# Kernel optimization log

Measured on AMD Instinct MI355X. Metric: run time of the kernel, lower is better.

The kernel has to match this reference:

```python
import jax, jax.numpy as jnp
import numpy as np

NEG = -1e9  # mask value for non-edges (matches masked_fill(-inf) numerically-safely)
SLOPE = 0.2  # LeakyReLU negative slope in GraphAttentionLayer


def gat_layer(x, W, a_l, a_r, adj, n_heads):
    """One GraphAttentionLayer (eval mode, is_concat=True).
    e[i,j,h] = leakyrelu(a_l . g[i,h] + a_r . g[j,h])  (attn Linear split into halves)
    softmax over j masked by adj, then aggregate neighbors.
    """
    n = x.shape[0]
    g = (x @ W).reshape(n, n_heads, -1)          # [n, h, f]
    el = jnp.einsum('ihf,f->ih', g, a_l)          # score contribution of node i
    er = jnp.einsum('jhf,f->jh', g, a_r)          # score contribution of node j
    e = jax.nn.leaky_relu(el[:, None, :] + er[None, :, :], SLOPE)  # [n, n, h]
    e = jnp.where(adj[:, :, None] != 0, e, NEG)
    a = jax.nn.softmax(e, axis=1)                 # softmax over neighbors j
    out = jnp.einsum('ijh,jhf->ihf', a, g)        # weighted aggregation
    return out.reshape(n, -1)                     # concat heads


def setup_inputs() -> dict:
    key = jax.random.key(0)
    ks = jax.random.split(key, 8)
    N, IN, HID, OUT, H = 2048, 512, 256, 128, 8
    x = jax.random.normal(ks[0], (N, IN), dtype=jnp.float32)
    adj = jax.random.randint(ks[1], (N, N), 0, 2, dtype=jnp.int32)
    adj = adj.at[jnp.arange(N), jnp.arange(N)].set(1)  # self loops: no empty softmax rows
    s = 0.05
    W1 = jax.random.normal(ks[2], (IN, HID), dtype=jnp.float32) * s
    a1_l = jax.random.normal(ks[3], (HID // H,), dtype=jnp.float32) * s
    a1_r = jax.random.normal(ks[4], (HID // H,), dtype=jnp.float32) * s
    W2 = jax.random.normal(ks[5], (HID, OUT), dtype=jnp.float32) * s
    a2_l = jax.random.normal(ks[6], (OUT,), dtype=jnp.float32) * s
    a2_r = jax.random.normal(ks[7], (OUT,), dtype=jnp.float32) * s
    return {"x": x, "W1": W1, "a1_l": a1_l, "a1_r": a1_r,
            "W2": W2, "a2_l": a2_l, "a2_r": a2_r, "adj_mat": adj}


def reference(x, W1, a1_l, a1_r, W2, a2_l, a2_r, adj_mat):
    # eval mode: nn.Dropout is identity
    h = gat_layer(x, W1, a1_l, a1_r, adj_mat, n_heads=8)
    h = jax.nn.elu(h)
    out = gat_layer(h, W2, a2_l, a2_r, adj_mat, n_heads=1)
    return out
```

## Files before the change

kernel.cpp:

```cpp
#include <hip/hip_runtime.h>
#include <hip/hip_bf16.h>

#define NN 2048
typedef unsigned short u16;
typedef unsigned long long u64;
typedef __attribute__((ext_vector_type(8))) short short8;
typedef __attribute__((ext_vector_type(4))) float f32x4;

__device__ __forceinline__ unsigned bfb(float x) {
    unsigned u = __float_as_uint(x);
    return (u + 0x7FFFu + ((u >> 16) & 1u)) >> 16;
}
__device__ __forceinline__ unsigned pk2(float a, float b) { return bfb(a) | (bfb(b) << 16); }

__global__ __launch_bounds__(256) void prep(const float* __restrict__ x,
                                            const float* __restrict__ W1,
                                            const float* __restrict__ W2,
                                            const int* __restrict__ adj,
                                            u16* __restrict__ xb, u16* __restrict__ w1t,
                                            u16* __restrict__ w2t, u64* __restrict__ ab) {
    const int b = blockIdx.x;
    if (b < 16384) {
        int t = b * 256 + threadIdx.x;
        int W = t >> 6, lane = t & 63;
        int i = W >> 5, jw = W & 31;
        int a = adj[(size_t)i * NN + jw * 64 + lane];
        u64 m = __ballot(a != 0);
        if (lane == 0) ab[(size_t)i * 32 + jw] = m;
    } else if (b < 16384 + 1024) {
        int t = (b - 16384) * 256 + threadIdx.x;
        float4 v = ((const float4*)x)[t];
        uint2 o;
        o.x = pk2(v.x, v.y);
        o.y = pk2(v.z, v.w);
        ((uint2*)xb)[t] = o;
    } else if (b < 16384 + 1024 + 512) {
        int u = (b - 17408) * 256 + threadIdx.x;
        int c = u >> 9, k = u & 511;
        w1t[u] = (u16)bfb(W1[(size_t)k * 256 + c]);
    } else {
        int u = (b - 17920) * 256 + threadIdx.x;
        int c = u >> 8, k = u & 255;
        w2t[u] = (u16)bfb(W2[(size_t)k * 128 + c]);
    }
}

__global__ __launch_bounds__(256) void gemm1(const u16* __restrict__ A,
                                             const u16* __restrict__ BT,
                                             const float* __restrict__ al,
                                             const float* __restrict__ ar,
                                             u16* __restrict__ GT,
                                             float* __restrict__ el,
                                             float* __restrict__ ert) {
    const int i0 = blockIdx.x * 16, cs = blockIdx.y;
    const int t = threadIdx.x, lane = t & 63, w = t >> 6;
    const int q = lane >> 4, n = lane & 15;
    const int ct = w & 1, kh = w >> 1;
    __shared__ float osh[2][16][16];
    __shared__ float pel[2][16], per_[2][16];

    const u16* ap = A + (size_t)(i0 + n) * 512 + kh * 256 + q * 8;
    const u16* bp = BT + (size_t)(cs * 32 + ct * 16 + n) * 512 + kh * 256 + q * 8;
    f32x4 acc = {0.f, 0.f, 0.f, 0.f};
#pragma unroll
    for (int ks = 0; ks < 8; ++ks) {
        short8 a = *(const short8*)(ap + ks * 32);
        short8 b = *(const short8*)(bp + ks * 32);
        acc = __builtin_amdgcn_mfma_f32_16x16x32_bf16(a, b, acc, 0, 0, 0);
    }
    if (kh == 1) {
#pragma unroll
        for (int r = 0; r < 4; ++r) osh[ct][q * 4 + r][n] = acc[r];
    }
    __syncthreads();
    if (kh == 0) {
#pragma unroll
        for (int r = 0; r < 4; ++r) acc[r] += osh[ct][q * 4 + r][n];
        uint2 g0;
        g0.x = pk2(acc[0], acc[1]);
        g0.y = pk2(acc[2], acc[3]);
        *(uint2*)&GT[(size_t)(cs * 32 + ct * 16 + n) * NN + i0 + q * 4] = g0;
        const float alv = al[ct * 16 + n], arv = ar[ct * 16 + n];
#pragma unroll
        for (int r = 0; r < 4; ++r) {
            float ve = acc[r] * alv, vr = acc[r] * arv;
#pragma unroll
            for (int off = 1; off <= 8; off <<= 1) {
                ve += __shfl_xor(ve, off);
                vr += __shfl_xor(vr, off);
            }
            if (n == 0) { pel[ct][q * 4 + r] = ve; per_[ct][q * 4 + r] = vr; }
        }
    }
    __syncthreads();
    if (t < 16) {
        el[(size_t)(i0 + t) * 8 + cs] = pel[0][t] + pel[1][t];
        ert[(size_t)cs * NN + i0 + t] = per_[0][t] + per_[1][t];
    }
}

__global__ __launch_bounds__(256) void gemm2(const u16* __restrict__ A,
                                             const u16* __restrict__ BT,
                                             const float* __restrict__ al,
                                             const float* __restrict__ ar,
                                             u16* __restrict__ GT,
                                             float* __restrict__ el2p,
                                             float* __restrict__ er2p) {
    const int i0 = blockIdx.x * 16, cs = blockIdx.y;
    const int t = threadIdx.x, lane = t & 63, w = t >> 6;
    const int q = lane >> 4, n = lane & 15;
    const int ct = w & 1, kh = w >> 1;
    __shared__ float osh[2][16][16];
    __shared__ float pel[2][16], per_[2][16];

    const u16* ap = A + (size_t)(i0 + n) * 256 + kh * 128 + q * 8;
    const u16* bp = BT + (size_t)(cs * 32 + ct * 16 + n) * 256 + kh * 128 + q * 8;
    f32x4 acc = {0.f, 0.f, 0.f, 0.f};
#pragma unroll
    for (int ks = 0; ks < 4; ++ks) {
        short8 a = *(const short8*)(ap + ks * 32);
        short8 b = *(const short8*)(bp + ks * 32);
        acc = __builtin_amdgcn_mfma_f32_16x16x32_bf16(a, b, acc, 0, 0, 0);
    }
    if (kh == 1) {
#pragma unroll
        for (int r = 0; r < 4; ++r) osh[ct][q * 4 + r][n] = acc[r];
    }
    __syncthreads();
    if (kh == 0) {
#pragma unroll
        for (int r = 0; r < 4; ++r) acc[r] += osh[ct][q * 4 + r][n];
        uint2 g0;
        g0.x = pk2(acc[0], acc[1]);
        g0.y = pk2(acc[2], acc[3]);
        *(uint2*)&GT[(size_t)(cs * 32 + ct * 16 + n) * NN + i0 + q * 4] = g0;
        const float alv = al[cs * 32 + ct * 16 + n], arv = ar[cs * 32 + ct * 16 + n];
#pragma unroll
        for (int r = 0; r < 4; ++r) {
            float ve = acc[r] * alv, vr = acc[r] * arv;
#pragma unroll
            for (int off = 1; off <= 8; off <<= 1) {
                ve += __shfl_xor(ve, off);
                vr += __shfl_xor(vr, off);
            }
            if (n == 0) { pel[ct][q * 4 + r] = ve; per_[ct][q * 4 + r] = vr; }
        }
    }
    __syncthreads();
    if (t < 16) {
        el2p[(size_t)cs * NN + i0 + t] = pel[0][t] + pel[1][t];
        er2p[(size_t)cs * NN + i0 + t] = per_[0][t] + per_[1][t];
    }
}

__global__ __launch_bounds__(512) void attn1(const float* __restrict__ el,
                                             const float* __restrict__ ert,
                                             const unsigned* __restrict__ ab32,
                                             const u16* __restrict__ gbt,
                                             u16* __restrict__ hbb) {
    const int rt = blockIdx.x, sec = blockIdx.y;
    const int i0 = rt * 16, h0 = sec * 2;
    const int t = threadIdx.x, lane = t & 63, w = t >> 6;
    const int q = lane >> 4, n = lane & 15;
    const int m = t >> 5, jq = t & 31;
    const int hl = w >> 2, ch = (w >> 1) & 1, kf2 = w & 1;

    __shared__ u16 ersb[2][2048];
    __shared__ __align__(16) u16 pl[2][2][16][136];
    __shared__ unsigned absh[16][64];
    __shared__ float psum_sh[16][2];
    __shared__ float osh[2][2][16][16];
    __shared__ float wmax[2][8];
    __shared__ float mxsh[2];

    float4 v0 = *(const float4*)(ert + (size_t)h0 * NN + t * 4);
    float4 v1 = *(const float4*)(ert + (size_t)(h0 + 1) * NN + t * 4);
    uint2 c0, c1;
    c0.x = pk2(v0.x, v0.y); c0.y = pk2(v0.z, v0.w);
    c1.x = pk2(v1.x, v1.y); c1.y = pk2(v1.z, v1.w);
    *(uint2*)&ersb[0][t * 4] = c0;
    *(uint2*)&ersb[1][t * 4] = c1;
    float m0 = fmaxf(fmaxf(v0.x, v0.y), fmaxf(v0.z, v0.w));
    float m1 = fmaxf(fmaxf(v1.x, v1.y), fmaxf(v1.z, v1.w));
#pragma unroll
    for (int off = 32; off; off >>= 1) {
        m0 = fmaxf(m0, __shfl_xor(m0, off));
        m1 = fmaxf(m1, __shfl_xor(m1, off));
    }
    if (lane == 0) { wmax[0][w] = m0; wmax[1][w] = m1; }
    for (int c = t; c < 1024; c += 512)
        absh[c >> 6][c & 63] = ab32[(size_t)(i0 + (c >> 6)) * 64 + (c & 63)];
    __syncthreads();
    if (t < 2) {
        float mm = wmax[t][0];
#pragma unroll
        for (int ww = 1; ww < 8; ++ww) mm = fmaxf(mm, wmax[t][ww]);
        mxsh[t] = mm;
    }
    __syncthreads();

    float elv[2], mxv[2], ps[2];
#pragma unroll
    for (int h = 0; h < 2; ++h) {
        float e = el[(size_t)(i0 + m) * 8 + h0 + h];
        elv[h] = e;
        float mm = e + mxsh[h];
        mxv[h] = fmaxf(mm, 0.2f * mm);
        ps[h] = 0.f;
    }

    auto stage = [&](int tl, int nb) {
        unsigned word = absh[m][tl * 4 + (jq >> 3)];
        unsigned bits = (word >> ((jq & 7) * 4)) & 0xFu;
        const int jo = tl * 128 + jq * 4;
        uint2 raw0 = *(const uint2*)&ersb[0][jo];
        uint2 raw1 = *(const uint2*)&ersb[1][jo];
#pragma unroll
        for (int h = 0; h < 2; ++h) {
            uint2 raw = h ? raw1 : raw0;
            float e0 = __uint_as_float(raw.x << 16);
            float e1 = __uint_as_float(raw.x & 0xFFFF0000u);
            float e2 = __uint_as_float(raw.y << 16);
            float e3 = __uint_as_float(raw.y & 0xFFFF0000u);
            float s0 = elv[h] + e0, s1 = elv[h] + e1, s2 = elv[h] + e2, s3 = elv[h] + e3;
            s0 = fmaxf(s0, 0.2f * s0) - mxv[h];
            s1 = fmaxf(s1, 0.2f * s1) - mxv[h];
            s2 = fmaxf(s2, 0.2f * s2) - mxv[h];
            s3 = fmaxf(s3, 0.2f * s3) - mxv[h];
            float p0 = (bits & 1u) ? __expf(s0) : 0.f;
            float p1 = (bits & 2u) ? __expf(s1) : 0.f;
            float p2 = (bits & 4u) ? __expf(s2) : 0.f;
            float p3 = (bits & 8u) ? __expf(s3) : 0.f;
            ps[h] += (p0 + p1) + (p2 + p3);
            uint2 pkv;
            pkv.x = pk2(p0, p1);
            pkv.y = pk2(p2, p3);
            *(uint2*)&pl[nb][h][m][jq * 4] = pkv;
        }
    };

    const int col = sec * 64 + hl * 32 + ch * 16 + n;
    const u16* gb = gbt + (size_t)col * NN + kf2 * 64 + q * 8;
    short8 bc0 = *(const short8*)gb;
    short8 bc1 = *(const short8*)(gb + 32);
    f32x4 acc = {0.f, 0.f, 0.f, 0.f};

    stage(0, 0);
    __syncthreads();

    for (int tile = 0; tile < 16; ++tile) {
        short8 bn0 = bc0, bn1 = bc1;
        if (tile < 15) {
            bn0 = *(const short8*)(gb + tile * 128 + 128);
            bn1 = *(const short8*)(gb + tile * 128 + 160);
        }
        const u16* ap = &pl[tile & 1][hl][n][kf2 * 64 + q * 8];
        short8 a0 = *(const short8*)ap;
        short8 a1 = *(const short8*)(ap + 32);
        acc = __builtin_amdgcn_mfma_f32_16x16x32_bf16(a0, bc0, acc, 0, 0, 0);
        acc = __builtin_amdgcn_mfma_f32_16x16x32_bf16(a1, bc1, acc, 0, 0, 0);
        if (tile < 15) stage(tile + 1, (tile + 1) & 1);
        bc0 = bn0; bc1 = bn1;
        __syncthreads();
    }

#pragma unroll
    for (int h = 0; h < 2; ++h) {
        float v = ps[h];
#pragma unroll
        for (int off = 16; off; off >>= 1) v += __shfl_down(v, off, 32);
        if (jq == 0) psum_sh[m][h] = v;
    }
    if (kf2 == 1) {
#pragma unroll
        for (int r = 0; r < 4; ++r) osh[hl][ch][q * 4 + r][n] = acc[r];
    }
    __syncthreads();
    if (kf2 == 0) {
#pragma unroll
        for (int r = 0; r < 4; ++r) {
            int mr = q * 4 + r;
            float o = (acc[r] + osh[hl][ch][mr][n]) / psum_sh[mr][hl];
            o = o > 0.f ? o : (__expf(o) - 1.f);
            hbb[(size_t)(i0 + mr) * 256 + col] = (u16)bfb(o);
        }
    }
}

__global__ __launch_bounds__(512) void attn2(const float* __restrict__ el2p,
                                             const float* __restrict__ er2p,
                                             const unsigned* __restrict__ ab32,
                                             const u16* __restrict__ gbt,
                                             float* __restrict__ out) {
    const int rt = blockIdx.x, sec = blockIdx.y;
    const int i0 = rt * 16;
    const int t = threadIdx.x, lane = t & 63, w = t >> 6;
    const int q = lane >> 4, n = lane & 15;
    const int m = t >> 5, jq = t & 31;
    const int ct = w >> 1, kf2 = w & 1;

    __shared__ u16 ersb[2048];
    __shared__ __align__(16) u16 pl[2][16][136];
    __shared__ unsigned absh[16][64];
    __shared__ float psum_sh[16];
    __shared__ float osh[4][16][16];
    __shared__ float wmax[8];
    __shared__ float mxsh;

    float4 a0 = *(const float4*)(er2p + t * 4);
    float4 a1 = *(const float4*)(er2p + NN + t * 4);
    float4 a2 = *(const float4*)(er2p + 2 * NN + t * 4);
    float4 a3 = *(const float4*)(er2p + 3 * NN + t * 4);
    float4 v0;
    v0.x = ((a0.x + a1.x) + (a2.x + a3.x));
    v0.y = ((a0.y + a1.y) + (a2.y + a3.y));
    v0.z = ((a0.z + a1.z) + (a2.z + a3.z));
    v0.w = ((a0.w + a1.w) + (a2.w + a3.w));
    uint2 c0;
    c0.x = pk2(v0.x, v0.y); c0.y = pk2(v0.z, v0.w);
    *(uint2*)&ersb[t * 4] = c0;
    float m0 = fmaxf(fmaxf(v0.x, v0.y), fmaxf(v0.z, v0.w));
#pragma unroll
    for (int off = 32; off; off >>= 1) m0 = fmaxf(m0, __shfl_xor(m0, off));
    if (lane == 0) wmax[w] = m0;
    for (int c = t; c < 1024; c += 512)
        absh[c >> 6][c & 63] = ab32[(size_t)(i0 + (c >> 6)) * 64 + (c & 63)];
    __syncthreads();
    if (t == 0) {
        float mm = wmax[0];
#pragma unroll
        for (int ww = 1; ww < 8; ++ww) mm = fmaxf(mm, wmax[ww]);
        mxsh = mm;
    }
    __syncthreads();

    const float elv = el2p[i0 + m] + el2p[NN + i0 + m] + el2p[2 * NN + i0 + m] + el2p[3 * NN + i0 + m];
    float mm2 = elv + mxsh;
    const float mxv = fmaxf(mm2, 0.2f * mm2);
    float ps = 0.f;

    auto stage = [&](int tl, int nb) {
        unsigned word = absh[m][tl * 4 + (jq >> 3)];
        unsigned bits = (word >> ((jq & 7) * 4)) & 0xFu;
        const int jo = tl * 128 + jq * 4;
        uint2 raw = *(const uint2*)&ersb[jo];
        float e0 = __uint_as_float(raw.x << 16);
        float e1 = __uint_as_float(raw.x & 0xFFFF0000u);
        float e2 = __uint_as_float(raw.y << 16);
        float e3 = __uint_as_float(raw.y & 0xFFFF0000u);
        float s0 = elv + e0, s1 = elv + e1, s2 = elv + e2, s3 = elv + e3;
        s0 = fmaxf(s0, 0.2f * s0) - mxv;
        s1 = fmaxf(s1, 0.2f * s1) - mxv;
        s2 = fmaxf(s2, 0.2f * s2) - mxv;
        s3 = fmaxf(s3, 0.2f * s3) - mxv;
        float p0 = (bits & 1u) ? __expf(s0) : 0.f;
        float p1 = (bits & 2u) ? __expf(s1) : 0.f;
        float p2 = (bits & 4u) ? __expf(s2) : 0.f;
        float p3 = (bits & 8u) ? __expf(s3) : 0.f;
        ps += (p0 + p1) + (p2 + p3);
        uint2 pkv;
        pkv.x = pk2(p0, p1);
        pkv.y = pk2(p2, p3);
        *(uint2*)&pl[nb][m][jq * 4] = pkv;
    };

    const int col = sec * 64 + ct * 16 + n;
    const u16* gb = gbt + (size_t)col * NN + kf2 * 64 + q * 8;
    short8 bc0 = *(const short8*)gb;
    short8 bc1 = *(const short8*)(gb + 32);
    f32x4 acc = {0.f, 0.f, 0.f, 0.f};

    stage(0, 0);
    __syncthreads();

    for (int tile = 0; tile < 16; ++tile) {
        short8 bn0 = bc0, bn1 = bc1;
        if (tile < 15) {
            bn0 = *(const short8*)(gb + tile * 128 + 128);
            bn1 = *(const short8*)(gb + tile * 128 + 160);
        }
        const u16* ap = &pl[tile & 1][n][kf2 * 64 + q * 8];
        short8 a0v = *(const short8*)ap;
        short8 a1v = *(const short8*)(ap + 32);
        acc = __builtin_amdgcn_mfma_f32_16x16x32_bf16(a0v, bc0, acc, 0, 0, 0);
        acc = __builtin_amdgcn_mfma_f32_16x16x32_bf16(a1v, bc1, acc, 0, 0, 0);
        if (tile < 15) stage(tile + 1, (tile + 1) & 1);
        bc0 = bn0; bc1 = bn1;
        __syncthreads();
    }

#pragma unroll
    for (int off = 16; off; off >>= 1) ps += __shfl_down(ps, off, 32);
    if (jq == 0) psum_sh[m] = ps;
    if (kf2 == 1) {
#pragma unroll
        for (int r = 0; r < 4; ++r) osh[ct][q * 4 + r][n] = acc[r];
    }
    __syncthreads();
    if (kf2 == 0) {
#pragma unroll
        for (int r = 0; r < 4; ++r) {
            int mr = q * 4 + r;
            out[(size_t)(i0 + mr) * 128 + col] = (acc[r] + osh[ct][mr][n]) / psum_sh[mr];
        }
    }
}

extern "C" void kernel_launch(void* const* d_in, const int* in_sizes, int n_in,
                              void* d_out, int out_size, void* d_ws, size_t ws_size,
                              hipStream_t stream) {
    const float* x   = (const float*)d_in[0];
    const float* W1  = (const float*)d_in[1];
    const float* a1l = (const float*)d_in[2];
    const float* a1r = (const float*)d_in[3];
    const float* W2  = (const float*)d_in[4];
    const float* a2l = (const float*)d_in[5];
    const float* a2r = (const float*)d_in[6];
    const int* adj = (const int*)d_in[7];

    char* p = (char*)d_ws;
    u16* xb    = (u16*)p;            p += (size_t)NN * 512 * 2;
    u16* w1t   = (u16*)p;            p += (size_t)256 * 512 * 2;
    u16* w2t   = (u16*)p;            p += (size_t)128 * 256 * 2;
    unsigned* abits = (unsigned*)p;  p += (size_t)NN * 64 * 4;
    u16* gbt1  = (u16*)p;            p += (size_t)256 * NN * 2;
    u16* hbb   = (u16*)p;            p += (size_t)NN * 256 * 2;
    u16* gbt2  = (u16*)p;            p += (size_t)128 * NN * 2;
    float* el1 = (float*)p;          p += (size_t)NN * 8 * 4;
    float* ert1 = (float*)p;         p += (size_t)8 * NN * 4;
    float* el2p = (float*)p;         p += (size_t)4 * NN * 4;
    float* er2p = (float*)p;         p += (size_t)4 * NN * 4;

    prep<<<18048, 256, 0, stream>>>(x, W1, W2, adj, xb, w1t, w2t, (u64*)abits);

    gemm1<<<dim3(128, 8), 256, 0, stream>>>(xb, w1t, a1l, a1r, gbt1, el1, ert1);
    attn1<<<dim3(128, 4), 512, 0, stream>>>(el1, ert1, abits, gbt1, hbb);

    gemm2<<<dim3(128, 4), 256, 0, stream>>>(hbb, w2t, a2l, a2r, gbt2, el2p, er2p);
    attn2<<<dim3(128, 2), 512, 0, stream>>>(el2p, er2p, abits, gbt2, (float*)d_out);
}
```

Before: 128.6 us.

## Widen attention K-tiles, coarsen prep blocks, use hardware bf16 pack

The attention kernels now process 256 neighbour columns per tile instead of 128. That halves the loop iterations and the block-wide barriers, and issues four MFMAs per step instead of two, at the cost of larger shared buffers and more live registers. The prep kernel now has each block handle 4-8 chunks, cutting the grid from about 18k blocks to about 2.5k. The bf16 pair pack now uses the v_cvt_pk_bf16_f32 instruction instead of manual rounding, and attn1 gets a min-blocks launch bound of 4.

Measured after the change: 126.2 us. Within noise of the previous version (-1.9%).

```diff
diff --git a/kernel.cpp b/kernel.cpp
--- a/kernel.cpp
+++ b/kernel.cpp
@@ -11,7 +11,11 @@
     unsigned u = __float_as_uint(x);
     return (u + 0x7FFFu + ((u >> 16) & 1u)) >> 16;
 }
-__device__ __forceinline__ unsigned pk2(float a, float b) { return bfb(a) | (bfb(b) << 16); }
+__device__ __forceinline__ unsigned pk2(float a, float b) {
+    unsigned r;
+    asm("v_cvt_pk_bf16_f32 %0, %1, %2" : "=v"(r) : "v"(a), "v"(b));
+    return r;
+}
 
 __global__ __launch_bounds__(256) void prep(const float* __restrict__ x,
                                             const float* __restrict__ W1,
@@ -20,28 +24,41 @@
                                             u16* __restrict__ xb, u16* __restrict__ w1t,
                                             u16* __restrict__ w2t, u64* __restrict__ ab) {
     const int b = blockIdx.x;
-    if (b < 16384) {
-        int t = b * 256 + threadIdx.x;
-        int W = t >> 6, lane = t & 63;
-        int i = W >> 5, jw = W & 31;
-        int a = adj[(size_t)i * NN + jw * 64 + lane];
-        u64 m = __ballot(a != 0);
-        if (lane == 0) ab[(size_t)i * 32 + jw] = m;
-    } else if (b < 16384 + 1024) {
-        int t = (b - 16384) * 256 + threadIdx.x;
-        float4 v = ((const float4*)x)[t];
-        uint2 o;
-        o.x = pk2(v.x, v.y);
-        o.y = pk2(v.z, v.w);
-        ((uint2*)xb)[t] = o;
-    } else if (b < 16384 + 1024 + 512) {
-        int u = (b - 17408) * 256 + threadIdx.x;
-        int c = u >> 9, k = u & 511;
-        w1t[u] = (u16)bfb(W1[(size_t)k * 256 + c]);
+    const int tid = threadIdx.x;
+    if (b < 2048) {
+#pragma unroll
+        for (int k = 0; k < 8; ++k) {
+            int t = (b * 8 + k) * 256 + tid;
+            int W = t >> 6, lane = t & 63;
+            int i = W >> 5, jw = W & 31;
+            int a = adj[(size_t)i * NN + jw * 64 + lane];
+            u64 mk = __ballot(a != 0);
+            if (lane == 0) ab[(size_t)i * 32 + jw] = mk;
+        }
+    } else if (b < 2048 + 256) {
+#pragma unroll
+        for (int k = 0; k < 4; ++k) {
+            int t = ((b - 2048) * 4 + k) * 256 + tid;
+            float4 v = ((const float4*)x)[t];
+            uint2 o;
+            o.x = pk2(v.x, v.y);
+            o.y = pk2(v.z, v.w);
+            ((uint2*)xb)[t] = o;
+        }
+    } else if (b < 2048 + 256 + 128) {
+#pragma unroll
+        for (int k = 0; k < 4; ++k) {
+            int u = ((b - 2304) * 4 + k) * 256 + tid;
+            int c = u >> 9, kk = u & 511;
+            w1t[u] = (u16)bfb(W1[(size_t)kk * 256 + c]);
+        }
     } else {
-        int u = (b - 17920) * 256 + threadIdx.x;
-        int c = u >> 8, k = u & 255;
-        w2t[u] = (u16)bfb(W2[(size_t)k * 128 + c]);
+#pragma unroll
+        for (int k = 0; k < 4; ++k) {
+            int u = ((b - 2432) * 4 + k) * 256 + tid;
+            int c = u >> 8, kk = u & 255;
+            w2t[u] = (u16)bfb(W2[(size_t)kk * 128 + c]);
+        }
     }
 }
 
@@ -153,11 +170,11 @@
     }
 }
 
-__global__ __launch_bounds__(512) void attn1(const float* __restrict__ el,
-                                             const float* __restrict__ ert,
-                                             const unsigned* __restrict__ ab32,
-                                             const u16* __restrict__ gbt,
-                                             u16* __restrict__ hbb) {
+__global__ __launch_bounds__(512, 4) void attn1(const float* __restrict__ el,
+                                                const float* __restrict__ ert,
+                                                const unsigned* __restrict__ ab32,
+                                                const u16* __restrict__ gbt,
+                                                u16* __restrict__ hbb) {
     const int rt = blockIdx.x, sec = blockIdx.y;
     const int i0 = rt * 16, h0 = sec * 2;
     const int t = threadIdx.x, lane = t & 63, w = t >> 6;
@@ -166,7 +183,7 @@
     const int hl = w >> 2, ch = (w >> 1) & 1, kf2 = w & 1;
 
     __shared__ u16 ersb[2][2048];
-    __shared__ __align__(16) u16 pl[2][2][16][136];
+    __shared__ __align__(16) u16 pl[2][2][16][264];
     __shared__ unsigned absh[16][64];
     __shared__ float psum_sh[16][2];
     __shared__ float osh[2][2][16][16];
@@ -210,57 +227,69 @@
     }
 
     auto stage = [&](int tl, int nb) {
-        unsigned word = absh[m][tl * 4 + (jq >> 3)];
-        unsigned bits = (word >> ((jq & 7) * 4)) & 0xFu;
-        const int jo = tl * 128 + jq * 4;
-        uint2 raw0 = *(const uint2*)&ersb[0][jo];
-        uint2 raw1 = *(const uint2*)&ersb[1][jo];
-#pragma unroll
-        for (int h = 0; h < 2; ++h) {
-            uint2 raw = h ? raw1 : raw0;
-            float e0 = __uint_as_float(raw.x << 16);
-            float e1 = __uint_as_float(raw.x & 0xFFFF0000u);
-            float e2 = __uint_as_float(raw.y << 16);
-            float e3 = __uint_as_float(raw.y & 0xFFFF0000u);
-            float s0 = elv[h] + e0, s1 = elv[h] + e1, s2 = elv[h] + e2, s3 = elv[h] + e3;
-            s0 = fmaxf(s0, 0.2f * s0) - mxv[h];
-            s1 = fmaxf(s1, 0.2f * s1) - mxv[h];
-            s2 = fmaxf(s2, 0.2f * s2) - mxv[h];
-            s3 = fmaxf(s3, 0.2f * s3) - mxv[h];
-            float p0 = (bits & 1u) ? __expf(s0) : 0.f;
-            float p1 = (bits & 2u) ? __expf(s1) : 0.f;
-            float p2 = (bits & 4u) ? __expf(s2) : 0.f;
-            float p3 = (bits & 8u) ? __expf(s3) : 0.f;
-            ps[h] += (p0 + p1) + (p2 + p3);
-            uint2 pkv;
-            pkv.x = pk2(p0, p1);
-            pkv.y = pk2(p2, p3);
-            *(uint2*)&pl[nb][h][m][jq * 4] = pkv;
+#pragma unroll
+        for (int sub = 0; sub < 2; ++sub) {
+            unsigned word = absh[m][tl * 8 + sub * 4 + (jq >> 3)];
+            unsigned bits = (word >> ((jq & 7) * 4)) & 0xFu;
+            const int jo = tl * 256 + sub * 128 + jq * 4;
+            uint2 raw0 = *(const uint2*)&ersb[0][jo];
+            uint2 raw1 = *(const uint2*)&ersb[1][jo];
+#pragma unroll
+            for (int h = 0; h < 2; ++h) {
+                uint2 raw = h ? raw1 : raw0;
+                float e0 = __uint_as_float(raw.x << 16);
+                float e1 = __uint_as_float(raw.x & 0xFFFF0000u);
+                float e2 = __uint_as_float(raw.y << 16);
+                float e3 = __uint_as_float(raw.y & 0xFFFF0000u);
+                float s0 = elv[h] + e0, s1 = elv[h] + e1, s2 = elv[h] + e2, s3 = elv[h] + e3;
+                s0 = fmaxf(s0, 0.2f * s0) - mxv[h];
+                s1 = fmaxf(s1, 0.2f * s1) - mxv[h];
+                s2 = fmaxf(s2, 0.2f * s2) - mxv[h];
+                s3 = fmaxf(s3, 0.2f * s3) - mxv[h];
+                float p0 = (bits & 1u) ? __expf(s0) : 0.f;
+                float p1 = (bits & 2u) ? __expf(s1) : 0.f;
+                float p2 = (bits & 4u) ? __expf(s2) : 0.f;
+                float p3 = (bits & 8u) ? __expf(s3) : 0.f;
+                ps[h] += (p0 + p1) + (p2 + p3);
+                uint2 pkv;
+                pkv.x = pk2(p0, p1);
+                pkv.y = pk2(p2, p3);
+                *(uint2*)&pl[nb][h][m][sub * 128 + jq * 4] = pkv;
+            }
         }
     };
 
     const int col = sec * 64 + hl * 32 + ch * 16 + n;
-    const u16* gb = gbt + (size_t)col * NN + kf2 * 64 + q * 8;
+    const u16* gb = gbt + (size_t)col * NN + kf2 * 128 + q * 8;
     short8 bc0 = *(const short8*)gb;
     short8 bc1 = *(const short8*)(gb + 32);
+    short8 bc2 = *(const short8*)(gb + 64);
+    short8 bc3 = *(const short8*)(gb + 96);
     f32x4 acc = {0.f, 0.f, 0.f, 0.f};
 
     stage(0, 0);
     __syncthreads();
 
-    for (int tile = 0; tile < 16; ++tile) {
-        short8 bn0 = bc0, bn1 = bc1;
-        if (tile < 15) {
-            bn0 = *(const short8*)(gb + tile * 128 + 128);
-            bn1 = *(const short8*)(gb + tile * 128 + 160);
-        }
-        const u16* ap = &pl[tile & 1][hl][n][kf2 * 64 + q * 8];
+    for (int tile = 0; tile < 8; ++tile) {
+        short8 bn0 = bc0, bn1 = bc1, bn2 = bc2, bn3 = bc3;
+        if (tile < 7) {
+            const u16* gq = gb + (tile + 1) * 256;
+            bn0 = *(const short8*)gq;
+            bn1 = *(const short8*)(gq + 32);
+            bn2 = *(const short8*)(gq + 64);
+            bn3 = *(const short8*)(gq + 96);
+        }
+        const u16* ap = &pl[tile & 1][hl][n][kf2 * 128 + q * 8];
         short8 a0 = *(const short8*)ap;
         short8 a1 = *(const short8*)(ap + 32);
+        short8 a2 = *(const short8*)(ap + 64);
+        short8 a3 = *(const short8*)(ap + 96);
         acc = __builtin_amdgcn_mfma_f32_16x16x32_bf16(a0, bc0, acc, 0, 0, 0);
         acc = __builtin_amdgcn_mfma_f32_16x16x32_bf16(a1, bc1, acc, 0, 0, 0);
-        if (tile < 15) stage(tile + 1, (tile + 1) & 1);
-        bc0 = bn0; bc1 = bn1;
+        acc = __builtin_amdgcn_mfma_f32_16x16x32_bf16(a2, bc2, acc, 0, 0, 0);
+        acc = __builtin_amdgcn_mfma_f32_16x16x32_bf16(a3, bc3, acc, 0, 0, 0);
+        if (tile < 7) stage(tile + 1, (tile + 1) & 1);
+        bc0 = bn0; bc1 = bn1; bc2 = bn2; bc3 = bn3;
         __syncthreads();
     }
 
@@ -300,7 +329,7 @@
     const int ct = w >> 1, kf2 = w & 1;
 
     __shared__ u16 ersb[2048];
-    __shared__ __align__(16) u16 pl[2][16][136];
+    __shared__ __align__(16) u16 pl[2][16][264];
     __shared__ unsigned absh[16][64];
     __shared__ float psum_sh[16];
     __shared__ float osh[4][16][16];
@@ -340,52 +369,64 @@
     float ps = 0.f;
 
     auto stage = [&](int tl, int nb) {
-        unsigned word = absh[m][tl * 4 + (jq >> 3)];
-        unsigned bits = (word >> ((jq & 7) * 4)) & 0xFu;
-        const int jo = tl * 128 + jq * 4;
-        uint2 raw = *(const uint2*)&ersb[jo];
-        float e0 = __uint_as_float(raw.x << 16);
-        float e1 = __uint_as_float(raw.x & 0xFFFF0000u);
-        float e2 = __uint_as_float(raw.y << 16);
-        float e3 = __uint_as_float(raw.y & 0xFFFF0000u);
-        float s0 = elv + e0, s1 = elv + e1, s2 = elv + e2, s3 = elv + e3;
-        s0 = fmaxf(s0, 0.2f * s0) - mxv;
-        s1 = fmaxf(s1, 0.2f * s1) - mxv;
-        s2 = fmaxf(s2, 0.2f * s2) - mxv;
-        s3 = fmaxf(s3, 0.2f * s3) - mxv;
-        float p0 = (bits & 1u) ? __expf(s0) : 0.f;
-        float p1 = (bits & 2u) ? __expf(s1) : 0.f;
-        float p2 = (bits & 4u) ? __expf(s2) : 0.f;
-        float p3 = (bits & 8u) ? __expf(s3) : 0.f;
-        ps += (p0 + p1) + (p2 + p3);
-        uint2 pkv;
-        pkv.x = pk2(p0, p1);
-        pkv.y = pk2(p2, p3);
-        *(uint2*)&pl[nb][m][jq * 4] = pkv;
+#pragma unroll
+        for (int sub = 0; sub < 2; ++sub) {
+            unsigned word = absh[m][tl * 8 + sub * 4 + (jq >> 3)];
+            unsigned bits = (word >> ((jq & 7) * 4)) & 0xFu;
+            const int jo = tl * 256 + sub * 128 + jq * 4;
+            uint2 raw = *(const uint2*)&ersb[jo];
+            float e0 = __uint_as_float(raw.x << 16);
+            float e1 = __uint_as_float(raw.x & 0xFFFF0000u);
+            float e2 = __uint_as_float(raw.y << 16);
+            float e3 = __uint_as_float(raw.y & 0xFFFF0000u);
+            float s0 = elv + e0, s1 = elv + e1, s2 = elv + e2, s3 = elv + e3;
+            s0 = fmaxf(s0, 0.2f * s0) - mxv;
+            s1 = fmaxf(s1, 0.2f * s1) - mxv;
+            s2 = fmaxf(s2, 0.2f * s2) - mxv;
+            s3 = fmaxf(s3, 0.2f * s3) - mxv;
+            float p0 = (bits & 1u) ? __expf(s0) : 0.f;
+            float p1 = (bits & 2u) ? __expf(s1) : 0.f;
+            float p2 = (bits & 4u) ? __expf(s2) : 0.f;
+            float p3 = (bits & 8u) ? __expf(s3) : 0.f;
+            ps += (p0 + p1) + (p2 + p3);
+            uint2 pkv;
+            pkv.x = pk2(p0, p1);
+            pkv.y = pk2(p2, p3);
+            *(uint2*)&pl[nb][m][sub * 128 + jq * 4] = pkv;
+        }
     };
 
     const int col = sec * 64 + ct * 16 + n;
-    const u16* gb = gbt + (size_t)col * NN + kf2 * 64 + q * 8;
+    const u16* gb = gbt + (size_t)col * NN + kf2 * 128 + q * 8;
     short8 bc0 = *(const short8*)gb;
     short8 bc1 = *(const short8*)(gb + 32);
+    short8 bc2 = *(const short8*)(gb + 64);
+    short8 bc3 = *(const short8*)(gb + 96);
     f32x4 acc = {0.f, 0.f, 0.f, 0.f};
 
     stage(0, 0);
     __syncthreads();
 
-    for (int tile = 0; tile < 16; ++tile) {
-        short8 bn0 = bc0, bn1 = bc1;
-        if (tile < 15) {
-            bn0 = *(const short8*)(gb + tile * 128 + 128);
-            bn1 = *(const short8*)(gb + tile * 128 + 160);
-        }
-        const u16* ap = &pl[tile & 1][n][kf2 * 64 + q * 8];
+    for (int tile = 0; tile < 8; ++tile) {
+        short8 bn0 = bc0, bn1 = bc1, bn2 = bc2, bn3 = bc3;
+        if (tile < 7) {
+            const u16* gq = gb + (tile + 1) * 256;
+            bn0 = *(const short8*)gq;
+            bn1 = *(const short8*)(gq + 32);
+            bn2 = *(const short8*)(gq + 64);
+            bn3 = *(const short8*)(gq + 96);
+        }
+        const u16* ap = &pl[tile & 1][n][kf2 * 128 + q * 8];
         short8 a0v = *(const short8*)ap;
         short8 a1v = *(const short8*)(ap + 32);
+        short8 a2v = *(const short8*)(ap + 64);
+        short8 a3v = *(const short8*)(ap + 96);
         acc = __builtin_amdgcn_mfma_f32_16x16x32_bf16(a0v, bc0, acc, 0, 0, 0);
         acc = __builtin_amdgcn_mfma_f32_16x16x32_bf16(a1v, bc1, acc, 0, 0, 0);
-        if (tile < 15) stage(tile + 1, (tile + 1) & 1);
-        bc0 = bn0; bc1 = bn1;
+        acc = __builtin_amdgcn_mfma_f32_16x16x32_bf16(a2v, bc2, acc, 0, 0, 0);
+        acc = __builtin_amdgcn_mfma_f32_16x16x32_bf16(a3v, bc3, acc, 0, 0, 0);
+        if (tile < 7) stage(tile + 1, (tile + 1) & 1);
+        bc0 = bn0; bc1 = bn1; bc2 = bn2; bc3 = bn3;
         __syncthreads();
     }
 
@@ -431,7 +472,7 @@
     float* el2p = (float*)p;         p += (size_t)4 * NN * 4;
     float* er2p = (float*)p;         p += (size_t)4 * NN * 4;
 
-    prep<<<18048, 256, 0, stream>>>(x, W1, W2, adj, xb, w1t, w2t, (u64*)abits);
+    prep<<<2464, 256, 0, stream>>>(x, W1, W2, adj, xb, w1t, w2t, (u64*)abits);
 
     gemm1<<<dim3(128, 8), 256, 0, stream>>>(xb, w1t, a1l, a1r, gbt1, el1, ert1);
     attn1<<<dim3(128, 4), 512, 0, stream>>>(el1, ert1, abits, gbt1, hbb);
```
